# Kernel optimization log

Measured on AMD Instinct MI355X. Metric: run time of the kernel, lower is better.

The kernel has to match this reference:

```python
import math
import jax, jax.numpy as jnp
import numpy as np

TWO_PI = 2.0 * math.pi
LN_EPS = 1e-5


def wrap_angle(a):
    # wrap to (-pi, pi]
    return (a + math.pi) % TWO_PI - math.pi


def setup_inputs() -> dict:
    key = jax.random.key(0)
    ks = jax.random.split(key, 8)
    N = 2000          # num sources / targets (agents)
    E = 200000        # num edges
    D = 4             # input_dim (fixed by RelativeContextPositionEmbedding)
    NF = 64           # num_freq_bands
    H = 128           # hidden_dim
    F = 2 * NF + 1    # fourier feature width per input channel
    source = jax.random.normal(ks[0], (N, 3), jnp.float32)
    target = jax.random.normal(ks[1], (N, 5), jnp.float32)
    edge = jax.random.randint(ks[2], (2, E), 0, N, dtype=jnp.int32)
    freqs = jax.random.normal(ks[3], (D, NF), jnp.float32)          # nn.Embedding(D, NF).weight
    W1 = jax.random.normal(ks[4], (D, F, H), jnp.float32) * 0.02    # per-branch Linear1
    b1 = jnp.zeros((D, H), jnp.float32)
    gamma = jnp.ones((D, H), jnp.float32)                            # per-branch LayerNorm
    beta = jnp.zeros((D, H), jnp.float32)
    W2 = jax.random.normal(ks[5], (D, H, H), jnp.float32) * 0.02    # per-branch Linear2
    b2 = jnp.zeros((D, H), jnp.float32)
    return {"source": source, "target": target, "edge": edge, "freqs": freqs,
            "W1": W1, "b1": b1, "gamma": gamma, "beta": beta, "W2": W2, "b2": b2}


def _compute_feature(source, target, edge):
    src_pos, src_head = source[:, :2], source[:, 2]
    tgt_pos, tgt_head, tgt_speed = target[:, :2], target[:, 2], target[:, 3]
    e0, e1 = edge[0], edge[1]
    pd = src_pos[e0] - tgt_pos[e1]              # [E, 2]
    dx, dy = pd[:, 0], pd[:, 1]
    dh = wrap_angle(src_head[e0] - tgt_head[e1])
    ang = jnp.arctan2(dy, dx)
    tvx = tgt_speed * jnp.cos(tgt_head)
    tvy = tgt_speed * jnp.sin(tgt_head)
    closing = tvx[e1] * jnp.cos(ang) + tvy[e1] * jnp.sin(ang)
    return jnp.stack([dx, dy, dh, closing], axis=-1)  # [E, 4]


def reference(source, target, edge, freqs, W1, b1, gamma, beta, W2, b2):
    # feature computed under torch.no_grad() -> stop_gradient
    feat = jax.lax.stop_gradient(_compute_feature(source, target, edge))  # [E, D]
    x = feat[:, :, None] * freqs[None] * TWO_PI                            # [E, D, NF]
    x = jnp.concatenate([jnp.cos(x), jnp.sin(x), feat[:, :, None]], axis=-1)  # [E, D, F]
    # 4 small Linear -> LayerNorm -> ReLU -> Linear branches, vectorized over D
    h = jnp.einsum('edf,dfh->edh', x, W1) + b1                             # [E, D, H]
    mu = jnp.mean(h, axis=-1, keepdims=True)
    var = jnp.mean(jnp.square(h - mu), axis=-1, keepdims=True)
    h = (h - mu) * jax.lax.rsqrt(var + LN_EPS) * gamma + beta
    h = jax.nn.relu(h)
    y = jnp.einsum('edh,dhk->edk', h, W2) + b2                             # [E, D, H]
    return y.sum(axis=1)                                                   # [E, H]
```

## Files before the change

### kernel.cpp

```cpp
#include <hip/hip_runtime.h>
#include <hip/hip_bf16.h>
#include <math.h>

namespace {

typedef __attribute__((ext_vector_type(8))) short  short8;
typedef __attribute__((ext_vector_type(4))) float  float4v;

constexpr float PI_F     = 3.14159265358979323846f;
constexpr float TWO_PI_F = 6.28318530717958647692f;

__device__ __forceinline__ unsigned pack2(float a, float b) {
    __hip_bfloat162 h = __float22bfloat162_rn(float2{a, b});
    unsigned r;
    __builtin_memcpy(&r, &h, 4);
    return r;
}

union Frag {
    unsigned u[4];
    short8   s;
};

__device__ __forceinline__ void gl2lds16(const void* g, void* l) {
    __builtin_amdgcn_global_load_lds(
        (const __attribute__((address_space(1))) void*)g,
        (__attribute__((address_space(3))) void*)l, 16, 0, 0);
}

__global__ __launch_bounds__(256)
void prep_weights(const float* __restrict__ W1,
                  const float* __restrict__ W2,
                  ushort* __restrict__ W1T,
                  ushort* __restrict__ W2T) {
    const int idx = blockIdx.x * 256 + threadIdx.x;
    if (idx < 65536) {
        const int d = idx >> 14;
        const int n = (idx >> 7) & 127;
        const int k = idx & 127;
        __hip_bfloat16 v = __float2bfloat16(W1[(d * 129 + k) * 128 + n]);
        ushort u; __builtin_memcpy(&u, &v, 2);
        W1T[idx] = u;
    } else {
        const int j = idx - 65536;
        const int d = j >> 14;
        const int n = (j >> 7) & 127;
        const int kslot = j & 127;
        const int c = 32 * (kslot >> 5) + 16 * ((kslot >> 2) & 1)
                    + 4 * ((kslot >> 3) & 3) + (kslot & 3);
        __hip_bfloat16 v = __float2bfloat16(W2[(d * 128 + c) * 128 + n]);
        ushort u; __builtin_memcpy(&u, &v, 2);
        W2T[j] = u;
    }
}

__device__ __forceinline__ void stage_tile(const ushort* __restrict__ Wsrc,
                                           ushort* dst, int wv, int lane) {
    const int e4 = lane & 15;
    const int g  = lane >> 4;
    #pragma unroll
    for (int ks = 0; ks < 4; ++ks) {
        const ushort* gp = Wsrc + ((16 * wv + e4) * 128 + g * 8 + 32 * ks);
        gl2lds16(gp, dst + (wv * 4 + ks) * 512);
    }
}

__global__ __launch_bounds__(512, 4)
void rcpe_pipe(const float* __restrict__ source,
               const float* __restrict__ target,
               const int*   __restrict__ edge,
               const float* __restrict__ freqs,
               const float* __restrict__ W1,
               const ushort* __restrict__ W1T,
               const float* __restrict__ b1,
               const float* __restrict__ gamma,
               const float* __restrict__ beta,
               const ushort* __restrict__ W2T,
               const float* __restrict__ b2,
               float* __restrict__ out,
               int E)
{
    __shared__ __align__(16) ushort wbuf[2][16384];
    __shared__ __align__(16) float b1_lds[4][128];
    __shared__ __align__(16) float gm_lds[4][128];
    __shared__ __align__(16) float bt_lds[4][128];
    __shared__ __align__(16) float w1r_lds[4][128];
    __shared__ __align__(16) float feat_lds[4][128];
    __shared__ __align__(16) float freq_lds[4][64];

    const int tid  = threadIdx.x;
    const int wv   = tid >> 6;
    const int lane = tid & 63;
    const int e4   = lane & 15;
    const int g    = lane >> 4;
    const int ebase = blockIdx.x * 128;
    const int eg    = ebase + wv * 16 + e4;

    stage_tile(W1T, wbuf[0], wv, lane);

    {
        const int dd = tid >> 7, c = tid & 127;
        b1_lds[dd][c]  = b1[tid];
        gm_lds[dd][c]  = gamma[tid];
        bt_lds[dd][c]  = beta[tid];
        w1r_lds[dd][c] = W1[(dd * 129 + 128) * 128 + c];
    }
    if (tid < 256) ((float*)freq_lds)[tid] = freqs[tid];

    if (tid < 128) {
        const int e  = ebase + tid;
        const int ec = (e < E) ? e : (E - 1);
        const int s_i = edge[ec];
        const int t_i = edge[E + ec];
        const float sx = source[s_i * 3 + 0];
        const float sy = source[s_i * 3 + 1];
        const float sh = source[s_i * 3 + 2];
        const float tx = target[t_i * 5 + 0];
        const float ty = target[t_i * 5 + 1];
        const float th = target[t_i * 5 + 2];
        const float ts = target[t_i * 5 + 3];
        const float dx = sx - tx;
        const float dy = sy - ty;
        float a = sh - th + PI_F;
        a = fmodf(a, TWO_PI_F);
        if (a < 0.0f) a += TWO_PI_F;
        const float dh  = a - PI_F;
        const float ang = atan2f(dy, dx);
        const float tvx = ts * cosf(th);
        const float tvy = ts * sinf(th);
        const float closing = tvx * cosf(ang) + tvy * sinf(ang);
        feat_lds[0][tid] = dx;
        feat_lds[1][tid] = dy;
        feat_lds[2][tid] = dh;
        feat_lds[3][tid] = closing;
    }

    float4v y[8];
    #pragma unroll
    for (int t = 0; t < 8; ++t) {
        float4v a = {0.f, 0.f, 0.f, 0.f};
        #pragma unroll
        for (int d = 0; d < 4; ++d) {
            const float4v bv = *(const float4v*)(b2 + d * 128 + 16 * t + 4 * g);
            #pragma unroll
            for (int r = 0; r < 4; ++r) a[r] += bv[r];
        }
        y[t] = a;
    }

    __syncthreads();

    #pragma unroll 1
    for (int d = 0; d < 4; ++d) {
        stage_tile(W2T + d * 16384, wbuf[1], wv, lane);

        const float fe = feat_lds[d][wv * 16 + e4];

        Frag xf[4];
        {
            float cl[8], sl[8], ch8[8], sh8[8];
            #pragma unroll
            for (int j = 0; j < 8; ++j) {
                const float frL = freq_lds[d][8 * g + j];
                const float frH = freq_lds[d][32 + 8 * g + j];
                const float tL = __builtin_amdgcn_fractf(fe * frL);
                const float tH = __builtin_amdgcn_fractf(fe * frH);
                sl[j]  = __builtin_amdgcn_sinf(tL);
                cl[j]  = __builtin_amdgcn_cosf(tL);
                sh8[j] = __builtin_amdgcn_sinf(tH);
                ch8[j] = __builtin_amdgcn_cosf(tH);
            }
            #pragma unroll
            for (int p = 0; p < 4; ++p) {
                xf[0].u[p] = pack2(cl[2 * p],  cl[2 * p + 1]);
                xf[1].u[p] = pack2(ch8[2 * p], ch8[2 * p + 1]);
                xf[2].u[p] = pack2(sl[2 * p],  sl[2 * p + 1]);
                xf[3].u[p] = pack2(sh8[2 * p], sh8[2 * p + 1]);
            }
        }

        float4v hacc[8];
        #pragma unroll
        for (int t = 0; t < 8; ++t) {
            float4v acc = *(const float4v*)&b1_lds[d][16 * t + 4 * g];
            #pragma unroll
            for (int ks = 0; ks < 4; ++ks) {
                const short8 aw = *(const short8*)&wbuf[0][(t * 4 + ks) * 512 + lane * 8];
                acc = __builtin_amdgcn_mfma_f32_16x16x32_bf16(aw, xf[ks].s, acc, 0, 0, 0);
            }
            hacc[t] = acc;
        }

        #pragma unroll
        for (int t = 0; t < 8; ++t) {
            const float4v wv4 = *(const float4v*)&w1r_lds[d][16 * t + 4 * g];
            #pragma unroll
            for (int r = 0; r < 4; ++r)
                hacc[t][r] = fmaf(fe, wv4[r], hacc[t][r]);
        }

        __syncthreads();

        if (d < 3) stage_tile(W1T + (d + 1) * 16384, wbuf[0], wv, lane);

        float sm = 0.f, sq = 0.f;
        #pragma unroll
        for (int t = 0; t < 8; ++t) {
            #pragma unroll
            for (int r = 0; r < 4; ++r) {
                const float v = hacc[t][r];
                sm += v;
                sq = fmaf(v, v, sq);
            }
        }
        sm += __shfl_xor(sm, 16, 64);
        sq += __shfl_xor(sq, 16, 64);
        sm += __shfl_xor(sm, 32, 64);
        sq += __shfl_xor(sq, 32, 64);
        const float mu   = sm * (1.f / 128.f);
        const float var  = sq * (1.f / 128.f) - mu * mu;
        const float rinv = rsqrtf(var + 1e-5f);
        #pragma unroll
        for (int t = 0; t < 8; ++t) {
            const float4v gv = *(const float4v*)&gm_lds[d][16 * t + 4 * g];
            const float4v bv = *(const float4v*)&bt_lds[d][16 * t + 4 * g];
            #pragma unroll
            for (int r = 0; r < 4; ++r) {
                float v = (hacc[t][r] - mu) * rinv;
                v = fmaf(v, gv[r], bv[r]);
                hacc[t][r] = fmaxf(v, 0.f);
            }
        }

        Frag bfr[4];
        #pragma unroll
        for (int ks = 0; ks < 4; ++ks) {
            bfr[ks].u[0] = pack2(hacc[2 * ks][0],     hacc[2 * ks][1]);
            bfr[ks].u[1] = pack2(hacc[2 * ks][2],     hacc[2 * ks][3]);
            bfr[ks].u[2] = pack2(hacc[2 * ks + 1][0], hacc[2 * ks + 1][1]);
            bfr[ks].u[3] = pack2(hacc[2 * ks + 1][2], hacc[2 * ks + 1][3]);
        }

        #pragma unroll
        for (int t = 0; t < 8; ++t) {
            float4v acc = y[t];
            #pragma unroll
            for (int ks = 0; ks < 4; ++ks) {
                const short8 aw = *(const short8*)&wbuf[1][(t * 4 + ks) * 512 + lane * 8];
                acc = __builtin_amdgcn_mfma_f32_16x16x32_bf16(aw, bfr[ks].s, acc, 0, 0, 0);
            }
            y[t] = acc;
        }

        __syncthreads();
    }

    if (eg < E) {
        #pragma unroll
        for (int t = 0; t < 8; ++t) {
            *(float4v*)(out + eg * 128 + 16 * t + 4 * g) = y[t];
        }
    }
}

}

extern "C" void kernel_launch(void* const* d_in, const int* in_sizes, int n_in,
                              void* d_out, int out_size, void* d_ws, size_t ws_size,
                              hipStream_t stream) {
    const float* source = (const float*)d_in[0];
    const float* target = (const float*)d_in[1];
    const int*   edge   = (const int*)  d_in[2];
    const float* freqs  = (const float*)d_in[3];
    const float* W1     = (const float*)d_in[4];
    const float* b1     = (const float*)d_in[5];
    const float* gammap = (const float*)d_in[6];
    const float* betap  = (const float*)d_in[7];
    const float* W2     = (const float*)d_in[8];
    const float* b2     = (const float*)d_in[9];
    float* out = (float*)d_out;

    ushort* W1T = (ushort*)d_ws;
    ushort* W2T = (ushort*)((char*)d_ws + 131072);

    const int E = in_sizes[2] / 2;

    prep_weights<<<dim3(512), dim3(256), 0, stream>>>(W1, W2, W1T, W2T);

    const int nblocks = (E + 127) / 128;
    rcpe_pipe<<<dim3(nblocks), dim3(512), 0, stream>>>(
        source, target, edge, freqs, W1, W1T, b1, gammap, betap, W2T, b2, out, E);
}
```

Measured before the change: 113.7 us.

## Process two 16-edge groups per wave to reuse weight fragments across MFMAs

Halves the block to 256 threads, with each wave handling 32 edges as two 16-edge groups that share each LDS weight fragment load across two MFMAs. Tile staging is rewritten so each wave loads 8 chunks instead of 4. This cuts LDS read traffic per MFMA and adds independent MFMA chains for latency hiding. The cost is doubled accumulator register pressure (yA/yB, haccA/haccB), which lowers waves per SIMD and occupancy.

After: 121.2 us. 6.6% more time.

```diff
diff --git a/kernel.cpp b/kernel.cpp
--- a/kernel.cpp
+++ b/kernel.cpp
@@ -17,10 +17,7 @@
     return r;
 }
 
-union Frag {
-    unsigned u[4];
-    short8   s;
-};
+union Frag { unsigned u[4]; short8 s; };
 
 __device__ __forceinline__ void gl2lds16(const void* g, void* l) {
     __builtin_amdgcn_global_load_lds(
@@ -54,19 +51,22 @@
     }
 }
 
-__device__ __forceinline__ void stage_tile(const ushort* __restrict__ Wsrc,
-                                           ushort* dst, int wv, int lane) {
+__device__ __forceinline__ void stage_tile4(const ushort* __restrict__ Wtile,
+                                            ushort* dst, int wv, int lane) {
     const int e4 = lane & 15;
     const int g  = lane >> 4;
     #pragma unroll
-    for (int ks = 0; ks < 4; ++ks) {
-        const ushort* gp = Wsrc + ((16 * wv + e4) * 128 + g * 8 + 32 * ks);
-        gl2lds16(gp, dst + (wv * 4 + ks) * 512);
-    }
-}
-
-__global__ __launch_bounds__(512, 4)
-void rcpe_pipe(const float* __restrict__ source,
+    for (int i = 0; i < 8; ++i) {
+        const int c  = 8 * wv + i;
+        const int tt = c >> 2;
+        const int ks = c & 3;
+        const ushort* gp = Wtile + (16 * tt + e4) * 128 + g * 8 + 32 * ks;
+        gl2lds16(gp, dst + c * 512);
+    }
+}
+
+__global__ __launch_bounds__(256, 2)
+void rcpe_dual(const float* __restrict__ source,
                const float* __restrict__ target,
                const int*   __restrict__ edge,
                const float* __restrict__ freqs,
@@ -94,18 +94,21 @@
     const int e4   = lane & 15;
     const int g    = lane >> 4;
     const int ebase = blockIdx.x * 128;
-    const int eg    = ebase + wv * 16 + e4;
-
-    stage_tile(W1T, wbuf[0], wv, lane);
-
-    {
-        const int dd = tid >> 7, c = tid & 127;
-        b1_lds[dd][c]  = b1[tid];
-        gm_lds[dd][c]  = gamma[tid];
-        bt_lds[dd][c]  = beta[tid];
+    const int eg0   = ebase + wv * 32 + e4;
+    const int eg1   = eg0 + 16;
+
+    stage_tile4(W1T, wbuf[0], wv, lane);
+
+    #pragma unroll
+    for (int i = 0; i < 2; ++i) {
+        const int idx = tid + 256 * i;
+        const int dd = idx >> 7, c = idx & 127;
+        b1_lds[dd][c]  = b1[idx];
+        gm_lds[dd][c]  = gamma[idx];
+        bt_lds[dd][c]  = beta[idx];
         w1r_lds[dd][c] = W1[(dd * 129 + 128) * 128 + c];
     }
-    if (tid < 256) ((float*)freq_lds)[tid] = freqs[tid];
+    ((float*)freq_lds)[tid] = freqs[tid];
 
     if (tid < 128) {
         const int e  = ebase + tid;
@@ -135,7 +138,7 @@
         feat_lds[3][tid] = closing;
     }
 
-    float4v y[8];
+    float4v yA[8], yB[8];
     #pragma unroll
     for (int t = 0; t < 8; ++t) {
         float4v a = {0.f, 0.f, 0.f, 0.f};
@@ -145,19 +148,24 @@
             #pragma unroll
             for (int r = 0; r < 4; ++r) a[r] += bv[r];
         }
-        y[t] = a;
+        yA[t] = a;
+        yB[t] = a;
     }
 
     __syncthreads();
 
     #pragma unroll 1
     for (int d = 0; d < 4; ++d) {
-        stage_tile(W2T + d * 16384, wbuf[1], wv, lane);
-
-        const float fe = feat_lds[d][wv * 16 + e4];
-
-        Frag xf[4];
-        {
+        stage_tile4(W2T + d * 16384, wbuf[1], wv, lane);
+
+        const float feA = feat_lds[d][wv * 32 + e4];
+        const float feB = feat_lds[d][wv * 32 + 16 + e4];
+
+        Frag xfA[4], xfB[4];
+        #pragma unroll
+        for (int grp = 0; grp < 2; ++grp) {
+            const float fe = grp ? feB : feA;
+            Frag* xf = grp ? xfB : xfA;
             float cl[8], sl[8], ch8[8], sh8[8];
             #pragma unroll
             for (int j = 0; j < 8; ++j) {
@@ -179,87 +187,113 @@
             }
         }
 
-        float4v hacc[8];
-        #pragma unroll
-        for (int t = 0; t < 8; ++t) {
-            float4v acc = *(const float4v*)&b1_lds[d][16 * t + 4 * g];
+        float4v haccA[8], haccB[8];
+        #pragma unroll
+        for (int t = 0; t < 8; ++t) {
+            const float4v bv = *(const float4v*)&b1_lds[d][16 * t + 4 * g];
+            float4v accA = {bv[0], bv[1], bv[2], bv[3]};
+            float4v accB = accA;
             #pragma unroll
             for (int ks = 0; ks < 4; ++ks) {
                 const short8 aw = *(const short8*)&wbuf[0][(t * 4 + ks) * 512 + lane * 8];
-                acc = __builtin_amdgcn_mfma_f32_16x16x32_bf16(aw, xf[ks].s, acc, 0, 0, 0);
-            }
-            hacc[t] = acc;
+                accA = __builtin_amdgcn_mfma_f32_16x16x32_bf16(aw, xfA[ks].s, accA, 0, 0, 0);
+                accB = __builtin_amdgcn_mfma_f32_16x16x32_bf16(aw, xfB[ks].s, accB, 0, 0, 0);
+            }
+            haccA[t] = accA;
+            haccB[t] = accB;
         }
 
         #pragma unroll
         for (int t = 0; t < 8; ++t) {
             const float4v wv4 = *(const float4v*)&w1r_lds[d][16 * t + 4 * g];
             #pragma unroll
-            for (int r = 0; r < 4; ++r)
-                hacc[t][r] = fmaf(fe, wv4[r], hacc[t][r]);
+            for (int r = 0; r < 4; ++r) {
+                haccA[t][r] = fmaf(feA, wv4[r], haccA[t][r]);
+                haccB[t][r] = fmaf(feB, wv4[r], haccB[t][r]);
+            }
         }
 
         __syncthreads();
 
-        if (d < 3) stage_tile(W1T + (d + 1) * 16384, wbuf[0], wv, lane);
-
-        float sm = 0.f, sq = 0.f;
+        if (d < 3) stage_tile4(W1T + (d + 1) * 16384, wbuf[0], wv, lane);
+
+        float smA = 0.f, sqA = 0.f, smB = 0.f, sqB = 0.f;
         #pragma unroll
         for (int t = 0; t < 8; ++t) {
             #pragma unroll
             for (int r = 0; r < 4; ++r) {
-                const float v = hacc[t][r];
-                sm += v;
-                sq = fmaf(v, v, sq);
-            }
-        }
-        sm += __shfl_xor(sm, 16, 64);
-        sq += __shfl_xor(sq, 16, 64);
-        sm += __shfl_xor(sm, 32, 64);
-        sq += __shfl_xor(sq, 32, 64);
-        const float mu   = sm * (1.f / 128.f);
-        const float var  = sq * (1.f / 128.f) - mu * mu;
-        const float rinv = rsqrtf(var + 1e-5f);
+                const float vA = haccA[t][r];
+                const float vB = haccB[t][r];
+                smA += vA;  sqA = fmaf(vA, vA, sqA);
+                smB += vB;  sqB = fmaf(vB, vB, sqB);
+            }
+        }
+        smA += __shfl_xor(smA, 16, 64);
+        sqA += __shfl_xor(sqA, 16, 64);
+        smB += __shfl_xor(smB, 16, 64);
+        sqB += __shfl_xor(sqB, 16, 64);
+        smA += __shfl_xor(smA, 32, 64);
+        sqA += __shfl_xor(sqA, 32, 64);
+        smB += __shfl_xor(smB, 32, 64);
+        sqB += __shfl_xor(sqB, 32, 64);
+        const float muA   = smA * (1.f / 128.f);
+        const float muB   = smB * (1.f / 128.f);
+        const float rinvA = rsqrtf(sqA * (1.f / 128.f) - muA * muA + 1e-5f);
+        const float rinvB = rsqrtf(sqB * (1.f / 128.f) - muB * muB + 1e-5f);
         #pragma unroll
         for (int t = 0; t < 8; ++t) {
             const float4v gv = *(const float4v*)&gm_lds[d][16 * t + 4 * g];
             const float4v bv = *(const float4v*)&bt_lds[d][16 * t + 4 * g];
             #pragma unroll
             for (int r = 0; r < 4; ++r) {
-                float v = (hacc[t][r] - mu) * rinv;
-                v = fmaf(v, gv[r], bv[r]);
-                hacc[t][r] = fmaxf(v, 0.f);
-            }
-        }
-
-        Frag bfr[4];
+                float vA = (haccA[t][r] - muA) * rinvA;
+                float vB = (haccB[t][r] - muB) * rinvB;
+                vA = fmaf(vA, gv[r], bv[r]);
+                vB = fmaf(vB, gv[r], bv[r]);
+                haccA[t][r] = fmaxf(vA, 0.f);
+                haccB[t][r] = fmaxf(vB, 0.f);
+            }
+        }
+
+        Frag bfrA[4], bfrB[4];
         #pragma unroll
         for (int ks = 0; ks < 4; ++ks) {
-            bfr[ks].u[0] = pack2(hacc[2 * ks][0],     hacc[2 * ks][1]);
-            bfr[ks].u[1] = pack2(hacc[2 * ks][2],     hacc[2 * ks][3]);
-            bfr[ks].u[2] = pack2(hacc[2 * ks + 1][0], hacc[2 * ks + 1][1]);
-            bfr[ks].u[3] = pack2(hacc[2 * ks + 1][2], hacc[2 * ks + 1][3]);
-        }
-
-        #pragma unroll
-        for (int t = 0; t < 8; ++t) {
-            float4v acc = y[t];
+            bfrA[ks].u[0] = pack2(haccA[2 * ks][0],     haccA[2 * ks][1]);
+            bfrA[ks].u[1] = pack2(haccA[2 * ks][2],     haccA[2 * ks][3]);
+            bfrA[ks].u[2] = pack2(haccA[2 * ks + 1][0], haccA[2 * ks + 1][1]);
+            bfrA[ks].u[3] = pack2(haccA[2 * ks + 1][2], haccA[2 * ks + 1][3]);
+            bfrB[ks].u[0] = pack2(haccB[2 * ks][0],     haccB[2 * ks][1]);
+            bfrB[ks].u[1] = pack2(haccB[2 * ks][2],     haccB[2 * ks][3]);
+            bfrB[ks].u[2] = pack2(haccB[2 * ks + 1][0], haccB[2 * ks + 1][1]);
+            bfrB[ks].u[3] = pack2(haccB[2 * ks + 1][2], haccB[2 * ks + 1][3]);
+        }
+
+        #pragma unroll
+        for (int t = 0; t < 8; ++t) {
+            float4v accA = yA[t];
+            float4v accB = yB[t];
             #pragma unroll
             for (int ks = 0; ks < 4; ++ks) {
                 const short8 aw = *(const short8*)&wbuf[1][(t * 4 + ks) * 512 + lane * 8];
-                acc = __builtin_amdgcn_mfma_f32_16x16x32_bf16(aw, bfr[ks].s, acc, 0, 0, 0);
-            }
-            y[t] = acc;
+                accA = __builtin_amdgcn_mfma_f32_16x16x32_bf16(aw, bfrA[ks].s, accA, 0, 0, 0);
+                accB = __builtin_amdgcn_mfma_f32_16x16x32_bf16(aw, bfrB[ks].s, accB, 0, 0, 0);
+            }
+            yA[t] = accA;
+            yB[t] = accB;
         }
 
         __syncthreads();
     }
 
-    if (eg < E) {
-        #pragma unroll
-        for (int t = 0; t < 8; ++t) {
-            *(float4v*)(out + eg * 128 + 16 * t + 4 * g) = y[t];
-        }
+    if (eg0 < E) {
+        #pragma unroll
+        for (int t = 0; t < 8; ++t)
+            *(float4v*)(out + eg0 * 128 + 16 * t + 4 * g) = yA[t];
+    }
+    if (eg1 < E) {
+        #pragma unroll
+        for (int t = 0; t < 8; ++t)
+            *(float4v*)(out + eg1 * 128 + 16 * t + 4 * g) = yB[t];
     }
 }
 
@@ -288,6 +322,6 @@
     prep_weights<<<dim3(512), dim3(256), 0, stream>>>(W1, W2, W1T, W2T);
 
     const int nblocks = (E + 127) / 128;
-    rcpe_pipe<<<dim3(nblocks), dim3(512), 0, stream>>>(
+    rcpe_dual<<<dim3(nblocks), dim3(256), 0, stream>>>(
         source, target, edge, freqs, W1, W1T, b1, gammap, betap, W2T, b2, out, E);
 }
```

## Split hidden dimension across wave pairs, halving edges per block

Applied to the files above, without the earlier changes.

Each block now handles 64 edges instead of 128, and each pair of waves shares 16 edges, with each wave computing half of the 128 hidden units. LayerNorm statistics are combined across the pair through a small LDS buffer, and the partial second-layer outputs are summed through LDS before the store. The aim is to cut per-wave register pressure and serial MFMA work and to double the block count for better latency hiding. In exchange it adds extra syncs and LDS traffic, recomputes the sinusoid features in both waves of a pair, and drops the bounds checks, so it assumes E is a multiple of 64.

New measurement: 157.7 us. 1.39x slower.

```diff
diff --git a/kernel.cpp b/kernel.cpp
--- a/kernel.cpp
+++ b/kernel.cpp
@@ -17,10 +17,7 @@
     return r;
 }
 
-union Frag {
-    unsigned u[4];
-    short8   s;
-};
+union Frag { unsigned u[4]; short8 s; };
 
 __device__ __forceinline__ void gl2lds16(const void* g, void* l) {
     __builtin_amdgcn_global_load_lds(
@@ -54,49 +51,47 @@
     }
 }
 
-__device__ __forceinline__ void stage_tile(const ushort* __restrict__ Wsrc,
-                                           ushort* dst, int wv, int lane) {
-    const int e4 = lane & 15;
-    const int g  = lane >> 4;
-    #pragma unroll
-    for (int ks = 0; ks < 4; ++ks) {
-        const ushort* gp = Wsrc + ((16 * wv + e4) * 128 + g * 8 + 32 * ks);
-        gl2lds16(gp, dst + (wv * 4 + ks) * 512);
-    }
-}
-
 __global__ __launch_bounds__(512, 4)
-void rcpe_pipe(const float* __restrict__ source,
-               const float* __restrict__ target,
-               const int*   __restrict__ edge,
-               const float* __restrict__ freqs,
-               const float* __restrict__ W1,
-               const ushort* __restrict__ W1T,
-               const float* __restrict__ b1,
-               const float* __restrict__ gamma,
-               const float* __restrict__ beta,
-               const ushort* __restrict__ W2T,
-               const float* __restrict__ b2,
-               float* __restrict__ out,
-               int E)
+void rcpe_split(const float* __restrict__ source,
+                const float* __restrict__ target,
+                const int*   __restrict__ edge,
+                const float* __restrict__ freqs,
+                const float* __restrict__ W1,
+                const ushort* __restrict__ W1T,
+                const float* __restrict__ b1,
+                const float* __restrict__ gamma,
+                const float* __restrict__ beta,
+                const ushort* __restrict__ W2T,
+                const float* __restrict__ b2,
+                float* __restrict__ out,
+                int E)
 {
-    __shared__ __align__(16) ushort wbuf[2][16384];
+    __shared__ __align__(16) ushort wbufA[16384];
+    __shared__ __align__(16) ushort wbufB[16384];
     __shared__ __align__(16) float b1_lds[4][128];
     __shared__ __align__(16) float gm_lds[4][128];
     __shared__ __align__(16) float bt_lds[4][128];
     __shared__ __align__(16) float w1r_lds[4][128];
-    __shared__ __align__(16) float feat_lds[4][128];
+    __shared__ __align__(16) float feat_lds[4][64];
     __shared__ __align__(16) float freq_lds[4][64];
+    __shared__ __align__(16) float2 pbuf[8][16];
 
     const int tid  = threadIdx.x;
     const int wv   = tid >> 6;
     const int lane = tid & 63;
     const int e4   = lane & 15;
     const int g    = lane >> 4;
-    const int ebase = blockIdx.x * 128;
-    const int eg    = ebase + wv * 16 + e4;
-
-    stage_tile(W1T, wbuf[0], wv, lane);
+    const int hw   = wv & 1;
+    const int pr   = wv >> 1;
+    const int ebase = blockIdx.x * 64;
+    const int eg    = ebase + pr * 16 + e4;
+
+    #pragma unroll
+    for (int i = 0; i < 4; ++i) {
+        const int c = 4 * wv + i;
+        const ushort* gp = W1T + (16 * (c >> 2) + e4) * 128 + g * 8 + 32 * (c & 3);
+        gl2lds16(gp, wbufA + c * 512);
+    }
 
     {
         const int dd = tid >> 7, c = tid & 127;
@@ -107,11 +102,10 @@
     }
     if (tid < 256) ((float*)freq_lds)[tid] = freqs[tid];
 
-    if (tid < 128) {
-        const int e  = ebase + tid;
-        const int ec = (e < E) ? e : (E - 1);
-        const int s_i = edge[ec];
-        const int t_i = edge[E + ec];
+    if (tid < 64) {
+        const int e   = ebase + tid;
+        const int s_i = edge[e];
+        const int t_i = edge[E + e];
         const float sx = source[s_i * 3 + 0];
         const float sy = source[s_i * 3 + 1];
         const float sh = source[s_i * 3 + 2];
@@ -139,11 +133,13 @@
     #pragma unroll
     for (int t = 0; t < 8; ++t) {
         float4v a = {0.f, 0.f, 0.f, 0.f};
-        #pragma unroll
-        for (int d = 0; d < 4; ++d) {
-            const float4v bv = *(const float4v*)(b2 + d * 128 + 16 * t + 4 * g);
-            #pragma unroll
-            for (int r = 0; r < 4; ++r) a[r] += bv[r];
+        if (hw == 0) {
+            #pragma unroll
+            for (int d = 0; d < 4; ++d) {
+                const float4v bv = *(const float4v*)(b2 + d * 128 + 16 * t + 4 * g);
+                #pragma unroll
+                for (int r = 0; r < 4; ++r) a[r] += bv[r];
+            }
         }
         y[t] = a;
     }
@@ -152,9 +148,14 @@
 
     #pragma unroll 1
     for (int d = 0; d < 4; ++d) {
-        stage_tile(W2T + d * 16384, wbuf[1], wv, lane);
-
-        const float fe = feat_lds[d][wv * 16 + e4];
+        #pragma unroll
+        for (int i = 0; i < 4; ++i) {
+            const int c = 4 * wv + i;
+            const ushort* gp = W2T + d * 16384 + (16 * (c >> 2) + e4) * 128 + g * 8 + 32 * (c & 3);
+            gl2lds16(gp, wbufB + c * 512);
+        }
+
+        const float fe = feat_lds[d][pr * 16 + e4];
 
         Frag xf[4];
         {
@@ -179,36 +180,32 @@
             }
         }
 
-        float4v hacc[8];
-        #pragma unroll
-        for (int t = 0; t < 8; ++t) {
-            float4v acc = *(const float4v*)&b1_lds[d][16 * t + 4 * g];
+        float4v hacc[4];
+        #pragma unroll
+        for (int tl = 0; tl < 4; ++tl) {
+            float4v acc = *(const float4v*)&b1_lds[d][hw * 64 + 16 * tl + 4 * g];
             #pragma unroll
             for (int ks = 0; ks < 4; ++ks) {
-                const short8 aw = *(const short8*)&wbuf[0][(t * 4 + ks) * 512 + lane * 8];
+                const short8 aw = *(const short8*)&wbufA[((hw * 4 + tl) * 4 + ks) * 512 + lane * 8];
                 acc = __builtin_amdgcn_mfma_f32_16x16x32_bf16(aw, xf[ks].s, acc, 0, 0, 0);
             }
-            hacc[t] = acc;
-        }
-
-        #pragma unroll
-        for (int t = 0; t < 8; ++t) {
-            const float4v wv4 = *(const float4v*)&w1r_lds[d][16 * t + 4 * g];
+            hacc[tl] = acc;
+        }
+
+        #pragma unroll
+        for (int tl = 0; tl < 4; ++tl) {
+            const float4v wv4 = *(const float4v*)&w1r_lds[d][hw * 64 + 16 * tl + 4 * g];
             #pragma unroll
             for (int r = 0; r < 4; ++r)
-                hacc[t][r] = fmaf(fe, wv4[r], hacc[t][r]);
-        }
-
-        __syncthreads();
-
-        if (d < 3) stage_tile(W1T + (d + 1) * 16384, wbuf[0], wv, lane);
+                hacc[tl][r] = fmaf(fe, wv4[r], hacc[tl][r]);
+        }
 
         float sm = 0.f, sq = 0.f;
         #pragma unroll
-        for (int t = 0; t < 8; ++t) {
+        for (int tl = 0; tl < 4; ++tl) {
             #pragma unroll
             for (int r = 0; r < 4; ++r) {
-                const float v = hacc[t][r];
+                const float v = hacc[tl][r];
                 sm += v;
                 sq = fmaf(v, v, sq);
             }
@@ -217,37 +214,51 @@
         sq += __shfl_xor(sq, 16, 64);
         sm += __shfl_xor(sm, 32, 64);
         sq += __shfl_xor(sq, 32, 64);
-        const float mu   = sm * (1.f / 128.f);
-        const float var  = sq * (1.f / 128.f) - mu * mu;
+        if (g == 0) pbuf[wv][e4] = float2{sm, sq};
+
+        __syncthreads();
+
+        if (d < 3) {
+            #pragma unroll
+            for (int i = 0; i < 4; ++i) {
+                const int c = 4 * wv + i;
+                const ushort* gp = W1T + (d + 1) * 16384 + (16 * (c >> 2) + e4) * 128 + g * 8 + 32 * (c & 3);
+                gl2lds16(gp, wbufA + c * 512);
+            }
+        }
+
+        const float2 po = pbuf[wv ^ 1][e4];
+        const float mu   = (sm + po.x) * (1.f / 128.f);
+        const float var  = (sq + po.y) * (1.f / 128.f) - mu * mu;
         const float rinv = rsqrtf(var + 1e-5f);
         #pragma unroll
-        for (int t = 0; t < 8; ++t) {
-            const float4v gv = *(const float4v*)&gm_lds[d][16 * t + 4 * g];
-            const float4v bv = *(const float4v*)&bt_lds[d][16 * t + 4 * g];
+        for (int tl = 0; tl < 4; ++tl) {
+            const float4v gv = *(const float4v*)&gm_lds[d][hw * 64 + 16 * tl + 4 * g];
+            const float4v bv = *(const float4v*)&bt_lds[d][hw * 64 + 16 * tl + 4 * g];
             #pragma unroll
             for (int r = 0; r < 4; ++r) {
-                float v = (hacc[t][r] - mu) * rinv;
+                float v = (hacc[tl][r] - mu) * rinv;
                 v = fmaf(v, gv[r], bv[r]);
-                hacc[t][r] = fmaxf(v, 0.f);
-            }
-        }
-
-        Frag bfr[4];
-        #pragma unroll
-        for (int ks = 0; ks < 4; ++ks) {
-            bfr[ks].u[0] = pack2(hacc[2 * ks][0],     hacc[2 * ks][1]);
-            bfr[ks].u[1] = pack2(hacc[2 * ks][2],     hacc[2 * ks][3]);
-            bfr[ks].u[2] = pack2(hacc[2 * ks + 1][0], hacc[2 * ks + 1][1]);
-            bfr[ks].u[3] = pack2(hacc[2 * ks + 1][2], hacc[2 * ks + 1][3]);
+                hacc[tl][r] = fmaxf(v, 0.f);
+            }
+        }
+
+        Frag bfr[2];
+        #pragma unroll
+        for (int kk = 0; kk < 2; ++kk) {
+            bfr[kk].u[0] = pack2(hacc[2 * kk][0],     hacc[2 * kk][1]);
+            bfr[kk].u[1] = pack2(hacc[2 * kk][2],     hacc[2 * kk][3]);
+            bfr[kk].u[2] = pack2(hacc[2 * kk + 1][0], hacc[2 * kk + 1][1]);
+            bfr[kk].u[3] = pack2(hacc[2 * kk + 1][2], hacc[2 * kk + 1][3]);
         }
 
         #pragma unroll
         for (int t = 0; t < 8; ++t) {
             float4v acc = y[t];
             #pragma unroll
-            for (int ks = 0; ks < 4; ++ks) {
-                const short8 aw = *(const short8*)&wbuf[1][(t * 4 + ks) * 512 + lane * 8];
-                acc = __builtin_amdgcn_mfma_f32_16x16x32_bf16(aw, bfr[ks].s, acc, 0, 0, 0);
+            for (int kk = 0; kk < 2; ++kk) {
+                const short8 aw = *(const short8*)&wbufB[(t * 4 + hw * 2 + kk) * 512 + lane * 8];
+                acc = __builtin_amdgcn_mfma_f32_16x16x32_bf16(aw, bfr[kk].s, acc, 0, 0, 0);
             }
             y[t] = acc;
         }
@@ -255,10 +266,21 @@
         __syncthreads();
     }
 
-    if (eg < E) {
+    float4v* ybuf = (float4v*)wbufA;
+    if (hw == 1) {
+        #pragma unroll
+        for (int t = 0; t < 8; ++t)
+            ybuf[(pr * 8 + t) * 64 + lane] = y[t];
+    }
+    __syncthreads();
+    if (hw == 0) {
         #pragma unroll
         for (int t = 0; t < 8; ++t) {
-            *(float4v*)(out + eg * 128 + 16 * t + 4 * g) = y[t];
+            const float4v yo = ybuf[(pr * 8 + t) * 64 + lane];
+            float4v o;
+            #pragma unroll
+            for (int r = 0; r < 4; ++r) o[r] = y[t][r] + yo[r];
+            *(float4v*)(out + eg * 128 + 16 * t + 4 * g) = o;
         }
     }
 }
@@ -287,7 +309,7 @@
 
     prep_weights<<<dim3(512), dim3(256), 0, stream>>>(W1, W2, W1T, W2T);
 
-    const int nblocks = (E + 127) / 128;
-    rcpe_pipe<<<dim3(nblocks), dim3(512), 0, stream>>>(
+    const int nblocks = E / 64;
+    rcpe_split<<<dim3(nblocks), dim3(512), 0, stream>>>(
         source, target, edge, freqs, W1, W1T, b1, gammap, betap, W2T, b2, out, E);
 }
```
